# Kernel optimization log

Measured on AMD Instinct MI355X. Metric: run time of the kernel, lower is better.

The kernel has to match this reference:

```python
import jax, jax.numpy as jnp
import numpy as np

DT = 1e-3
TAU_SYN_INV = 50.0   # overridden in SeqNet.__init__
TAU_MEM_INV = 100.0  # norse default
V_TH = 1.0
EPS = 1e-5
H1 = 512
H2 = 512
NOUT = 10


def setup_inputs() -> dict:
    key = jax.random.key(0)
    ks = jax.random.split(key, 11)
    T, B, F = 100, 512, 784
    x = jax.random.normal(ks[0], (T, B, F), dtype=jnp.float32)
    # torch.nn.Linear init ~ U(-1/sqrt(fan_in), 1/sqrt(fan_in))
    def lin(k, out_d, in_d):
        bound = 1.0 / np.sqrt(in_d)
        kw, kb = jax.random.split(k)
        W = jax.random.uniform(kw, (out_d, in_d), jnp.float32, -bound, bound)
        b = jax.random.uniform(kb, (out_d,), jnp.float32, -bound, bound)
        return W, b
    W0, b0 = lin(ks[1], H1, F)
    W1, b1 = lin(ks[2], H2, H1)
    g0 = jnp.ones((H1,), jnp.float32)
    bt0 = jnp.zeros((H1,), jnp.float32)
    g1 = jnp.ones((H2,), jnp.float32)
    bt1 = jnp.zeros((H2,), jnp.float32)
    # norse LILinearCell: input_weights ~ randn / sqrt(hidden), no bias
    Wo = jax.random.normal(ks[3], (NOUT, H2), jnp.float32) / np.sqrt(H2)
    return {"x": x, "W0": W0, "b0": b0, "W1": W1, "b1": b1,
            "g0": g0, "bt0": bt0, "g1": g1, "bt1": bt1, "Wo": Wo}


def _bn(z, g, b):
    # BatchNorm1d in training mode: per-step batch statistics (biased var)
    m = jnp.mean(z, axis=0)
    v = jnp.var(z, axis=0)
    return g * (z - m) * jax.lax.rsqrt(v + EPS) + b


def _lif_step(v, i, cur):
    # norse lif_feed_forward_step, v_leak=0, v_reset=0
    v_dec = v + DT * TAU_MEM_INV * (-v + i)          # membrane decay + input current
    i_dec = i * (1.0 - DT * TAU_SYN_INV)             # synaptic decay
    z = (v_dec - V_TH > 0).astype(cur.dtype)         # heaviside spike
    v_new = (1.0 - z) * v_dec                        # reset to 0 on spike
    i_new = i_dec + cur                              # inject weighted input
    return z, v_new, i_new


def reference(x, W0, b0, W1, b1, g0, bt0, g1, bt1, Wo):
    T, B = x.shape[0], x.shape[1]
    xf = x.reshape(T, B, -1)

    def step(carry, xt):
        v0, i0, v1, i1, vo, io = carry
        cur0 = xt @ W0.T + b0                        # [B, H1]
        z0, v0, i0 = _lif_step(v0, i0, cur0)
        h0 = _bn(z0, g0, bt0)
        cur1 = h0 @ W1.T + b1                        # [B, H2]
        z1, v1, i1 = _lif_step(v1, i1, cur1)
        h1 = _bn(z1, g1, bt1)
        # norse LILinearCell (li_step): leaky integrator, returns v
        vo_new = vo + DT * TAU_MEM_INV * (-vo + io)  # [B, 10]
        io_new = io * (1.0 - DT * TAU_SYN_INV) + h1 @ Wo.T
        return (v0, i0, v1, i1, vo_new, io_new), vo_new

    z32 = lambda d: jnp.zeros((B, d), x.dtype)
    carry0 = (z32(W0.shape[0]), z32(W0.shape[0]),
              z32(W1.shape[0]), z32(W1.shape[0]),
              z32(Wo.shape[0]), z32(Wo.shape[0]))
    _, voltages = jax.lax.scan(step, carry0, xf)
    return voltages  # [T, B, 10]
```

## Files before the change

kernel.cpp:

```cpp
#include <hip/hip_runtime.h>
#include <stdint.h>

#define T_    100
#define B_    512
#define F_    784
#define FP_   800
#define H_    512
#define NOUT_ 10
#define R_    (T_*B_)
#define BH    (B_*H_)

typedef _Float16 f16x8 __attribute__((ext_vector_type(8)));
typedef float    f32x4 __attribute__((ext_vector_type(4)));

__device__ __forceinline__ void gload_lds16(const void* g, void* l) {
    __builtin_amdgcn_global_load_lds(
        (const __attribute__((address_space(1))) uint32_t*)g,
        (__attribute__((address_space(3))) uint32_t*)l, 16, 0, 0);
}

__global__ void convW_kernel(const float* __restrict__ W, _Float16* __restrict__ Wh,
                             _Float16* __restrict__ Wl, int K, int Kp, int n)
{
    int idx = blockIdx.x * 256 + threadIdx.x;
    if (idx >= n) return;
    int r = idx / Kp, k = idx - r * Kp;
    float v = (k < K) ? W[r * K + k] : 0.f;
    _Float16 h = (_Float16)v;
    Wh[idx] = h;
    Wl[idx] = (_Float16)(v - (float)h);
}

__global__ __launch_bounds__(256, 2) void gemm0_mfma(
    const float* __restrict__ X, const _Float16* __restrict__ Wh,
    const _Float16* __restrict__ Wl, const float* __restrict__ bias,
    float* __restrict__ C)
{
    __shared__ _Float16 L[2 * 4 * 4096];
    const int tid  = threadIdx.x;
    const int gl   = (blockIdx.x & 7) * 200 + (blockIdx.x >> 3);
    const int r0   = (gl >> 2) * 128;
    const int n0   = (gl & 3) * 128;
    const int lane = tid & 63;
    const int wm = (tid >> 7) & 1, wn = (tid >> 6) & 1;
    const int frow = lane & 15, fgrp = lane >> 4;

    const int brow = tid >> 2;
    const int bcol = (((tid & 3) ^ ((brow >> 1) & 3)) << 3);
    const _Float16* WhB = Wh + (size_t)(n0 + brow) * FP_ + bcol;
    const _Float16* WlB = Wl + (size_t)(n0 + brow) * FP_ + bcol;

    const int arow = tid >> 1, ahalf = tid & 1;
    const float* Xb = X + (size_t)(r0 + arow) * F_ + ahalf * 16;
    const int aoff = arow * 32;
    const int ac0  = (((ahalf * 2)     ^ ((arow >> 1) & 3)) << 3);
    const int ac1  = (((ahalf * 2 + 1) ^ ((arow >> 1) & 3)) << 3);

    f32x4 acc[4][4];
#pragma unroll
    for (int i = 0; i < 4; i++)
#pragma unroll
        for (int j = 0; j < 4; j++) acc[i][j] = f32x4{0.f, 0.f, 0.f, 0.f};

    auto stageB = [&](int buf, int kt) {
        _Float16* dh = L + buf * 16384 + 8192;
        _Float16* dl = L + buf * 16384 + 12288;
        gload_lds16(WhB + kt,            dh + tid * 8);
        gload_lds16(WhB + 64 * FP_ + kt, dh + 2048 + tid * 8);
        gload_lds16(WlB + kt,            dl + tid * 8);
        gload_lds16(WlB + 64 * FP_ + kt, dl + 2048 + tid * 8);
    };
    auto loadA = [&](float4* xa, int kt) {
#pragma unroll
        for (int j = 0; j < 4; j++) {
            int c = kt + ahalf * 16 + j * 4;
            xa[j] = (c < F_) ? *(const float4*)(Xb + kt + j * 4)
                             : make_float4(0.f, 0.f, 0.f, 0.f);
        }
    };
    auto writeA = [&](const float4* xa, int buf) {
        _Float16* dh = L + buf * 16384;
        _Float16* dl = L + buf * 16384 + 4096;
        const float* v = (const float*)xa;
        f16x8 h0, l0, h1, l1;
#pragma unroll
        for (int j = 0; j < 8; j++) {
            _Float16 a = (_Float16)v[j];
            h0[j] = a; l0[j] = (_Float16)(v[j] - (float)a);
            _Float16 b = (_Float16)v[8 + j];
            h1[j] = b; l1[j] = (_Float16)(v[8 + j] - (float)b);
        }
        *(f16x8*)(dh + aoff + ac0) = h0;
        *(f16x8*)(dh + aoff + ac1) = h1;
        *(f16x8*)(dl + aoff + ac0) = l0;
        *(f16x8*)(dl + aoff + ac1) = l1;
    };

    {
        stageB(0, 0);
        float4 xa[4];
        loadA(xa, 0);
        writeA(xa, 0);
    }
    __syncthreads();

    int cur = 0;
    for (int kt = 0; kt < FP_; kt += 32) {
        const int nxt = cur ^ 1;
        const bool has = (kt + 32) < FP_;
        float4 xa[4];
        if (has) { stageB(nxt, kt + 32); loadA(xa, kt + 32); }

        const _Float16* bp = L + cur * 16384;
        f16x8 ah[4], al[4], bh[4], bl[4];
#pragma unroll
        for (int mi = 0; mi < 4; mi++) {
            int row = wm * 64 + mi * 16 + frow;
            int off = row * 32 + ((fgrp ^ ((row >> 1) & 3)) << 3);
            ah[mi] = *(const f16x8*)(bp + off);
            al[mi] = *(const f16x8*)(bp + 4096 + off);
        }
#pragma unroll
        for (int ni = 0; ni < 4; ni++) {
            int row = wn * 64 + ni * 16 + frow;
            int off = row * 32 + ((fgrp ^ ((row >> 1) & 3)) << 3);
            bh[ni] = *(const f16x8*)(bp + 8192 + off);
            bl[ni] = *(const f16x8*)(bp + 12288 + off);
        }
#pragma unroll
        for (int mi = 0; mi < 4; mi++)
#pragma unroll
            for (int ni = 0; ni < 4; ni++) {
                acc[mi][ni] = __builtin_amdgcn_mfma_f32_16x16x32_f16(ah[mi], bh[ni], acc[mi][ni], 0, 0, 0);
                acc[mi][ni] = __builtin_amdgcn_mfma_f32_16x16x32_f16(ah[mi], bl[ni], acc[mi][ni], 0, 0, 0);
                acc[mi][ni] = __builtin_amdgcn_mfma_f32_16x16x32_f16(al[mi], bh[ni], acc[mi][ni], 0, 0, 0);
            }

        if (has) writeA(xa, nxt);
        __syncthreads();
        cur = nxt;
    }

#pragma unroll
    for (int ni = 0; ni < 4; ni++) {
        int col = n0 + wn * 64 + ni * 16 + frow;
        float bv = bias[col];
#pragma unroll
        for (int mi = 0; mi < 4; mi++) {
            int rbase = r0 + wm * 64 + mi * 16 + fgrp * 4;
#pragma unroll
            for (int p = 0; p < 4; p++)
                C[(size_t)(rbase + p) * H_ + col] = acc[mi][ni][p] + bv;
        }
    }
}

__global__ __launch_bounds__(256, 3) void gemm1_mfma(
    const _Float16* __restrict__ Zh, const float* __restrict__ W1,
    const float* __restrict__ alpha, const float* __restrict__ bW,
    float* __restrict__ C)
{
    __shared__ _Float16 L[2 * 3 * 4096];
    const int tid  = threadIdx.x;
    const int gl   = (blockIdx.x & 7) * 200 + (blockIdx.x >> 3);
    const int r0   = (gl >> 2) * 128;
    const int n0   = (gl & 3) * 128;
    const int tt   = r0 >> 9;
    const int lane = tid & 63;
    const int wm = (tid >> 7) & 1, wn = (tid >> 6) & 1;
    const int frow = lane & 15, fgrp = lane >> 4;

    const int arow = tid >> 2;
    const int acol = (((tid & 3) ^ ((arow >> 1) & 3)) << 3);
    const _Float16* ZhB = Zh + (size_t)(r0 + arow) * H_ + acol;

    const int brow = tid >> 1, bhalf = tid & 1;
    const float* W1B = W1 + (size_t)(n0 + brow) * H_ + bhalf * 16;
    const float* alB = alpha + tt * H_ + bhalf * 16;
    const int boff = brow * 32;
    const int bc0  = (((bhalf * 2)     ^ ((brow >> 1) & 3)) << 3);
    const int bc1  = (((bhalf * 2 + 1) ^ ((brow >> 1) & 3)) << 3);

    f32x4 acc[4][4];
#pragma unroll
    for (int i = 0; i < 4; i++)
#pragma unroll
        for (int j = 0; j < 4; j++) acc[i][j] = f32x4{0.f, 0.f, 0.f, 0.f};

    auto stageA = [&](int buf, int kt) {
        _Float16* d = L + buf * 12288;
        gload_lds16(ZhB + kt,           d + tid * 8);
        gload_lds16(ZhB + 64 * H_ + kt, d + 2048 + tid * 8);
    };
    auto loadB = [&](float4* wv, float4* av, int kt) {
#pragma unroll
        for (int j = 0; j < 4; j++) {
            wv[j] = *(const float4*)(W1B + kt + j * 4);
            av[j] = *(const float4*)(alB + kt + j * 4);
        }
    };
    auto writeB = [&](const float4* wv, const float4* av, int buf) {
        _Float16* dh = L + buf * 12288 + 4096;
        _Float16* dl = L + buf * 12288 + 8192;
        const float* w = (const float*)wv;
        const float* a = (const float*)av;
        f16x8 h0, l0, h1, l1;
#pragma unroll
        for (int j = 0; j < 8; j++) {
            float p0 = a[j] * w[j];
            _Float16 q0 = (_Float16)p0;
            h0[j] = q0; l0[j] = (_Float16)(p0 - (float)q0);
            float p1 = a[8 + j] * w[8 + j];
            _Float16 q1 = (_Float16)p1;
            h1[j] = q1; l1[j] = (_Float16)(p1 - (float)q1);
        }
        *(f16x8*)(dh + boff + bc0) = h0;
        *(f16x8*)(dh + boff + bc1) = h1;
        *(f16x8*)(dl + boff + bc0) = l0;
        *(f16x8*)(dl + boff + bc1) = l1;
    };

    {
        stageA(0, 0);
        float4 wv[4], av[4];
        loadB(wv, av, 0);
        writeB(wv, av, 0);
    }
    __syncthreads();

    int cur = 0;
    for (int kt = 0; kt < H_; kt += 32) {
        const int nxt = cur ^ 1;
        const bool has = (kt + 32) < H_;
        float4 wv[4], av[4];
        if (has) { stageA(nxt, kt + 32); loadB(wv, av, kt + 32); }

        const _Float16* bp = L + cur * 12288;
        f16x8 az[4], bh[4], bl[4];
#pragma unroll
        for (int mi = 0; mi < 4; mi++) {
            int row = wm * 64 + mi * 16 + frow;
            int off = row * 32 + ((fgrp ^ ((row >> 1) & 3)) << 3);
            az[mi] = *(const f16x8*)(bp + off);
        }
#pragma unroll
        for (int ni = 0; ni < 4; ni++) {
            int row = wn * 64 + ni * 16 + frow;
            int off = row * 32 + ((fgrp ^ ((row >> 1) & 3)) << 3);
            bh[ni] = *(const f16x8*)(bp + 4096 + off);
            bl[ni] = *(const f16x8*)(bp + 8192 + off);
        }
#pragma unroll
        for (int mi = 0; mi < 4; mi++)
#pragma unroll
            for (int ni = 0; ni < 4; ni++) {
                acc[mi][ni] = __builtin_amdgcn_mfma_f32_16x16x32_f16(az[mi], bh[ni], acc[mi][ni], 0, 0, 0);
                acc[mi][ni] = __builtin_amdgcn_mfma_f32_16x16x32_f16(az[mi], bl[ni], acc[mi][ni], 0, 0, 0);
            }

        if (has) writeB(wv, av, nxt);
        __syncthreads();
        cur = nxt;
    }

#pragma unroll
    for (int ni = 0; ni < 4; ni++) {
        int col = n0 + wn * 64 + ni * 16 + frow;
        float bv = bW[tt * H_ + col];
#pragma unroll
        for (int mi = 0; mi < 4; mi++) {
            int rbase = r0 + wm * 64 + mi * 16 + fgrp * 4;
#pragma unroll
            for (int p = 0; p < 4; p++)
                C[(size_t)(rbase + p) * H_ + col] = acc[mi][ni][p] + bv;
        }
    }
}

__global__ __launch_bounds__(512) void bw_kernel(
    const float* __restrict__ beta, const float* __restrict__ W1,
    const float* __restrict__ b1, float* __restrict__ bW)
{
    __shared__ float bs[512];
    const int t = blockIdx.x, n = threadIdx.x;
    bs[n] = beta[t * H_ + n];
    __syncthreads();
    const float* wr = W1 + (size_t)n * H_;
    float s = b1[n];
    for (int f = 0; f < H_; f += 4) {
        float4 w = *(const float4*)(wr + f);
        s = fmaf(bs[f],     w.x, s);
        s = fmaf(bs[f + 1], w.y, s);
        s = fmaf(bs[f + 2], w.z, s);
        s = fmaf(bs[f + 3], w.w, s);
    }
    bW[t * H_ + n] = s;
}

__global__ __launch_bounds__(256) void lif_kernel(
    const float* __restrict__ cur, _Float16* __restrict__ z)
{
    const int tid = blockIdx.x * 256 + threadIdx.x;
    float v = 0.f, ii = 0.f;
    const float* p = cur + tid;
    _Float16* q = z + tid;
    for (int t = 0; t < T_; t++) {
        float vd = __fadd_rn(v, __fmul_rn(0.1f, __fsub_rn(ii, v)));
        float id = __fmul_rn(ii, 0.95f);
        int zz = (vd > 1.0f) ? 1 : 0;
        v  = zz ? 0.f : vd;
        ii = __fadd_rn(id, p[(size_t)t * BH]);
        q[(size_t)t * BH] = (_Float16)zz;
    }
}

__global__ void bn_kernel(const _Float16* __restrict__ z,
                          const float* __restrict__ g, const float* __restrict__ bt,
                          float* __restrict__ alpha, float* __restrict__ beta)
{
    const int t = blockIdx.x, h = threadIdx.x;
    const _Float16* p = z + (size_t)t * BH + h;
    float fs = 0.f;
    for (int b = 0; b < B_; b++) fs += (float)p[(size_t)b * H_];
    float m   = fs * (1.0f / 512.0f);
    float var = __fsub_rn(m, __fmul_rn(m, m));
    float al  = g[h] / sqrtf(__fadd_rn(var, 1e-5f));
    float be  = __fsub_rn(bt[h], __fmul_rn(m, al));
    alpha[t * H_ + h] = al;
    beta [t * H_ + h] = be;
}

__global__ __launch_bounds__(256) void ugemm_kernel(
    const _Float16* __restrict__ Z, const float* __restrict__ alpha,
    const float* __restrict__ beta, const float* __restrict__ Wo,
    float* __restrict__ U)
{
    const int tid  = threadIdx.x;
    const int wave = tid >> 6, lane = tid & 63;
    const size_t r = (size_t)blockIdx.x * 4 + wave;
    const int t = (int)(r >> 9);
    const _Float16* zr = Z + r * 512;
    const float* alp = alpha + t * 512;
    const float* bet = beta  + t * 512;
    float acc[NOUT_];
#pragma unroll
    for (int o = 0; o < NOUT_; o++) acc[o] = 0.f;
#pragma unroll
    for (int jj = 0; jj < 8; jj++) {
        int j = jj * 64 + lane;
        float h = fmaf((float)zr[j], alp[j], bet[j]);
#pragma unroll
        for (int o = 0; o < NOUT_; o++) acc[o] = fmaf(h, Wo[o * 512 + j], acc[o]);
    }
#pragma unroll
    for (int o = 0; o < NOUT_; o++) {
        float v = acc[o];
#pragma unroll
        for (int off = 32; off; off >>= 1) v += __shfl_down(v, off, 64);
        if (lane == 0) U[r * NOUT_ + o] = v;
    }
}

__global__ void li_kernel(const float* __restrict__ U, float* __restrict__ out)
{
    const int tid = blockIdx.x * 256 + threadIdx.x;
    if (tid >= B_ * NOUT_) return;
    float vo = 0.f, io = 0.f;
    for (int t = 0; t < T_; t++) {
        vo = __fadd_rn(vo, __fmul_rn(0.1f, __fsub_rn(io, vo)));
        out[t * (B_ * NOUT_) + tid] = vo;
        io = __fadd_rn(__fmul_rn(io, 0.95f), U[t * (B_ * NOUT_) + tid]);
    }
}

extern "C" void kernel_launch(void* const* d_in, const int* in_sizes, int n_in,
                              void* d_out, int out_size, void* d_ws, size_t ws_size,
                              hipStream_t stream)
{
    const float* X   = (const float*)d_in[0];
    const float* W0  = (const float*)d_in[1];
    const float* b0  = (const float*)d_in[2];
    const float* W1  = (const float*)d_in[3];
    const float* b1  = (const float*)d_in[4];
    const float* g0  = (const float*)d_in[5];
    const float* bt0 = (const float*)d_in[6];
    const float* g1  = (const float*)d_in[7];
    const float* bt1 = (const float*)d_in[8];
    const float* Wo  = (const float*)d_in[9];
    float* out = (float*)d_out;

    char* w = (char*)d_ws;
    float*    CUR    = (float*)w;
    _Float16* Zh     = (_Float16*)(w + 104857600);
    float*    alpha0 = (float*)(w + 104857600 + 52428800);
    float*    beta0  = alpha0 + T_*H_;
    float*    alpha1 = beta0  + T_*H_;
    float*    beta1  = alpha1 + T_*H_;
    float*    bW     = beta1  + T_*H_;
    float*    U      = bW     + T_*H_;
    _Float16* W0h    = (_Float16*)(U + R_*NOUT_);
    _Float16* W0l    = W0h + 512*FP_;

    convW_kernel<<<(512*FP_+255)/256, 256, 0, stream>>>(W0, W0h, W0l, F_, FP_, 512*FP_);

    gemm0_mfma  <<<1600,  256, 0, stream>>>(X, W0h, W0l, b0, CUR);
    lif_kernel  <<<1024,  256, 0, stream>>>(CUR, Zh);
    bn_kernel   <<<100,   512, 0, stream>>>(Zh, g0, bt0, alpha0, beta0);
    bw_kernel   <<<100,   512, 0, stream>>>(beta0, W1, b1, bW);
    gemm1_mfma  <<<1600,  256, 0, stream>>>(Zh, W1, alpha0, bW, CUR);
    lif_kernel  <<<1024,  256, 0, stream>>>(CUR, Zh);
    bn_kernel   <<<100,   512, 0, stream>>>(Zh, g1, bt1, alpha1, beta1);
    ugemm_kernel<<<12800, 256, 0, stream>>>(Zh, alpha1, beta1, Wo, U);
    li_kernel   <<<20,    256, 0, stream>>>(U, out);
}
```

Baseline: 605.0 us.

## Triple-buffer async LDS loads in both GEMMs and split BN reduction across blocks

Both MFMA GEMMs now keep three LDS stages for the async-loaded operand and prefetch two k-tiles ahead. Fine-grained vmcnt/lgkmcnt waits and raw s_barrier replace __syncthreads, and the MFMA block runs at raised wave priority, all to hide global-load latency. The batch-norm statistics kernel, which used only 100 blocks, is split into an 800-block partial-sum pass and a small finalize pass to expose more parallelism. The added LDS drops gemm1 occupancy from 3 to 2 blocks per CU, and the hand-written wait counts must exactly match the number of outstanding loads.

```diff
diff --git a/kernel.cpp b/kernel.cpp
--- a/kernel.cpp
+++ b/kernel.cpp
@@ -36,7 +36,7 @@
     const _Float16* __restrict__ Wl, const float* __restrict__ bias,
     float* __restrict__ C)
 {
-    __shared__ _Float16 L[2 * 4 * 4096];
+    __shared__ _Float16 L[40960];
     const int tid  = threadIdx.x;
     const int gl   = (blockIdx.x & 7) * 200 + (blockIdx.x >> 3);
     const int r0   = (gl >> 2) * 128;
@@ -62,15 +62,15 @@
 #pragma unroll
         for (int j = 0; j < 4; j++) acc[i][j] = f32x4{0.f, 0.f, 0.f, 0.f};
 
-    auto stageB = [&](int buf, int kt) {
-        _Float16* dh = L + buf * 16384 + 8192;
-        _Float16* dl = L + buf * 16384 + 12288;
+    auto stageB = [&](int sbuf, int kt) {
+        _Float16* dh = L + 16384 + sbuf * 8192;
+        _Float16* dl = dh + 4096;
         gload_lds16(WhB + kt,            dh + tid * 8);
         gload_lds16(WhB + 64 * FP_ + kt, dh + 2048 + tid * 8);
         gload_lds16(WlB + kt,            dl + tid * 8);
         gload_lds16(WlB + 64 * FP_ + kt, dl + 2048 + tid * 8);
     };
-    auto loadA = [&](float4* xa, int kt) {
+    auto loadA = [&](float4 (&xa)[4], int kt) {
 #pragma unroll
         for (int j = 0; j < 4; j++) {
             int c = kt + ahalf * 16 + j * 4;
@@ -78,9 +78,9 @@
                              : make_float4(0.f, 0.f, 0.f, 0.f);
         }
     };
-    auto writeA = [&](const float4* xa, int buf) {
-        _Float16* dh = L + buf * 16384;
-        _Float16* dl = L + buf * 16384 + 4096;
+    auto writeA = [&](int abuf, const float4 (&xa)[4]) {
+        _Float16* dh = L + abuf * 8192;
+        _Float16* dl = dh + 4096;
         const float* v = (const float*)xa;
         f16x8 h0, l0, h1, l1;
 #pragma unroll
@@ -96,37 +96,38 @@
         *(f16x8*)(dl + aoff + ac1) = l1;
     };
 
-    {
-        stageB(0, 0);
-        float4 xa[4];
-        loadA(xa, 0);
-        writeA(xa, 0);
-    }
-    __syncthreads();
-
-    int cur = 0;
-    for (int kt = 0; kt < FP_; kt += 32) {
-        const int nxt = cur ^ 1;
-        const bool has = (kt + 32) < FP_;
-        float4 xa[4];
-        if (has) { stageB(nxt, kt + 32); loadA(xa, kt + 32); }
-
-        const _Float16* bp = L + cur * 16384;
+    float4 R0[4], R1[4];
+    stageB(0, 0);
+    stageB(1, 32);
+    loadA(R0, 0);
+    loadA(R1, 32);
+    writeA(0, R0);
+    asm volatile("s_waitcnt lgkmcnt(0)" ::: "memory");
+    __builtin_amdgcn_sched_barrier(0);
+    __builtin_amdgcn_s_barrier();
+    __builtin_amdgcn_sched_barrier(0);
+
+    auto body = [&](int k, int rbuf, int sbuf, float4 (&Rl)[4], float4 (&Rw)[4],
+                    bool pf, bool dw) {
+        if (pf) { stageB(sbuf, (k + 2) * 32); loadA(Rl, (k + 2) * 32); }
+        const _Float16* Ab = L + (k & 1) * 8192;
+        const _Float16* Bb = L + 16384 + rbuf * 8192;
         f16x8 ah[4], al[4], bh[4], bl[4];
 #pragma unroll
         for (int mi = 0; mi < 4; mi++) {
             int row = wm * 64 + mi * 16 + frow;
             int off = row * 32 + ((fgrp ^ ((row >> 1) & 3)) << 3);
-            ah[mi] = *(const f16x8*)(bp + off);
-            al[mi] = *(const f16x8*)(bp + 4096 + off);
+            ah[mi] = *(const f16x8*)(Ab + off);
+            al[mi] = *(const f16x8*)(Ab + 4096 + off);
         }
 #pragma unroll
         for (int ni = 0; ni < 4; ni++) {
             int row = wn * 64 + ni * 16 + frow;
             int off = row * 32 + ((fgrp ^ ((row >> 1) & 3)) << 3);
-            bh[ni] = *(const f16x8*)(bp + 8192 + off);
-            bl[ni] = *(const f16x8*)(bp + 12288 + off);
-        }
+            bh[ni] = *(const f16x8*)(Bb + off);
+            bl[ni] = *(const f16x8*)(Bb + 4096 + off);
+        }
+        __builtin_amdgcn_s_setprio(1);
 #pragma unroll
         for (int mi = 0; mi < 4; mi++)
 #pragma unroll
@@ -135,11 +136,24 @@
                 acc[mi][ni] = __builtin_amdgcn_mfma_f32_16x16x32_f16(ah[mi], bl[ni], acc[mi][ni], 0, 0, 0);
                 acc[mi][ni] = __builtin_amdgcn_mfma_f32_16x16x32_f16(al[mi], bh[ni], acc[mi][ni], 0, 0, 0);
             }
-
-        if (has) writeA(xa, nxt);
-        __syncthreads();
-        cur = nxt;
-    }
+        __builtin_amdgcn_s_setprio(0);
+        if (dw) writeA((k + 1) & 1, Rw);
+        asm volatile("s_waitcnt vmcnt(8)" ::: "memory");
+        asm volatile("s_waitcnt lgkmcnt(0)" ::: "memory");
+        __builtin_amdgcn_sched_barrier(0);
+        __builtin_amdgcn_s_barrier();
+        __builtin_amdgcn_sched_barrier(0);
+    };
+
+    int rb = 0;
+    for (int kp = 0; kp < 12; kp++) {
+        int k = kp * 2;
+        body(k,     rb, rb == 0 ? 2 : rb - 1, R0, R1, (k + 2) <= 24, true);
+        rb = (rb == 2) ? 0 : rb + 1;
+        body(k + 1, rb, rb == 0 ? 2 : rb - 1, R1, R0, (k + 3) <= 24, true);
+        rb = (rb == 2) ? 0 : rb + 1;
+    }
+    body(24, rb, 0, R0, R1, false, false);
 
 #pragma unroll
     for (int ni = 0; ni < 4; ni++) {
@@ -155,12 +169,12 @@
     }
 }
 
-__global__ __launch_bounds__(256, 3) void gemm1_mfma(
+__global__ __launch_bounds__(256, 2) void gemm1_mfma(
     const _Float16* __restrict__ Zh, const float* __restrict__ W1,
     const float* __restrict__ alpha, const float* __restrict__ bW,
     float* __restrict__ C)
 {
-    __shared__ _Float16 L[2 * 3 * 4096];
+    __shared__ _Float16 L[28672];
     const int tid  = threadIdx.x;
     const int gl   = (blockIdx.x & 7) * 200 + (blockIdx.x >> 3);
     const int r0   = (gl >> 2) * 128;
@@ -187,21 +201,21 @@
 #pragma unroll
         for (int j = 0; j < 4; j++) acc[i][j] = f32x4{0.f, 0.f, 0.f, 0.f};
 
-    auto stageA = [&](int buf, int kt) {
-        _Float16* d = L + buf * 12288;
+    auto stageA = [&](int sbuf, int kt) {
+        _Float16* d = L + sbuf * 4096;
         gload_lds16(ZhB + kt,           d + tid * 8);
         gload_lds16(ZhB + 64 * H_ + kt, d + 2048 + tid * 8);
     };
-    auto loadB = [&](float4* wv, float4* av, int kt) {
+    auto loadB = [&](float4 (&wv)[4], float4 (&av)[4], int kt) {
 #pragma unroll
         for (int j = 0; j < 4; j++) {
             wv[j] = *(const float4*)(W1B + kt + j * 4);
             av[j] = *(const float4*)(alB + kt + j * 4);
         }
     };
-    auto writeB = [&](const float4* wv, const float4* av, int buf) {
-        _Float16* dh = L + buf * 12288 + 4096;
-        _Float16* dl = L + buf * 12288 + 8192;
+    auto writeB = [&](int wbuf, const float4 (&wv)[4], const float4 (&av)[4]) {
+        _Float16* dh = L + 12288 + wbuf * 8192;
+        _Float16* dl = dh + 4096;
         const float* w = (const float*)wv;
         const float* a = (const float*)av;
         f16x8 h0, l0, h1, l1;
@@ -220,36 +234,37 @@
         *(f16x8*)(dl + boff + bc1) = l1;
     };
 
-    {
-        stageA(0, 0);
-        float4 wv[4], av[4];
-        loadB(wv, av, 0);
-        writeB(wv, av, 0);
-    }
-    __syncthreads();
-
-    int cur = 0;
-    for (int kt = 0; kt < H_; kt += 32) {
-        const int nxt = cur ^ 1;
-        const bool has = (kt + 32) < H_;
-        float4 wv[4], av[4];
-        if (has) { stageA(nxt, kt + 32); loadB(wv, av, kt + 32); }
-
-        const _Float16* bp = L + cur * 12288;
+    float4 Wv0[4], Av0[4], Wv1[4], Av1[4];
+    stageA(0, 0);
+    stageA(1, 32);
+    loadB(Wv0, Av0, 0);
+    loadB(Wv1, Av1, 32);
+    writeB(0, Wv0, Av0);
+    asm volatile("s_waitcnt lgkmcnt(0)" ::: "memory");
+    __builtin_amdgcn_sched_barrier(0);
+    __builtin_amdgcn_s_barrier();
+    __builtin_amdgcn_sched_barrier(0);
+
+    auto body = [&](int k, int rbuf, int sbuf, float4 (&Wl_)[4], float4 (&Al_)[4],
+                    float4 (&Ww_)[4], float4 (&Aw_)[4], bool pf, bool dw) {
+        if (pf) { stageA(sbuf, (k + 2) * 32); loadB(Wl_, Al_, (k + 2) * 32); }
+        const _Float16* Ab = L + rbuf * 4096;
+        const _Float16* Bb = L + 12288 + (k & 1) * 8192;
         f16x8 az[4], bh[4], bl[4];
 #pragma unroll
         for (int mi = 0; mi < 4; mi++) {
             int row = wm * 64 + mi * 16 + frow;
             int off = row * 32 + ((fgrp ^ ((row >> 1) & 3)) << 3);
-            az[mi] = *(const f16x8*)(bp + off);
+            az[mi] = *(const f16x8*)(Ab + off);
         }
 #pragma unroll
         for (int ni = 0; ni < 4; ni++) {
             int row = wn * 64 + ni * 16 + frow;
             int off = row * 32 + ((fgrp ^ ((row >> 1) & 3)) << 3);
-            bh[ni] = *(const f16x8*)(bp + 4096 + off);
-            bl[ni] = *(const f16x8*)(bp + 8192 + off);
-        }
+            bh[ni] = *(const f16x8*)(Bb + off);
+            bl[ni] = *(const f16x8*)(Bb + 4096 + off);
+        }
+        __builtin_amdgcn_s_setprio(1);
 #pragma unroll
         for (int mi = 0; mi < 4; mi++)
 #pragma unroll
@@ -257,11 +272,26 @@
                 acc[mi][ni] = __builtin_amdgcn_mfma_f32_16x16x32_f16(az[mi], bh[ni], acc[mi][ni], 0, 0, 0);
                 acc[mi][ni] = __builtin_amdgcn_mfma_f32_16x16x32_f16(az[mi], bl[ni], acc[mi][ni], 0, 0, 0);
             }
-
-        if (has) writeB(wv, av, nxt);
-        __syncthreads();
-        cur = nxt;
-    }
+        __builtin_amdgcn_s_setprio(0);
+        if (dw) writeB((k + 1) & 1, Ww_, Aw_);
+        asm volatile("s_waitcnt vmcnt(10)" ::: "memory");
+        asm volatile("s_waitcnt lgkmcnt(0)" ::: "memory");
+        __builtin_amdgcn_sched_barrier(0);
+        __builtin_amdgcn_s_barrier();
+        __builtin_amdgcn_sched_barrier(0);
+    };
+
+    int rb = 0;
+    for (int kp = 0; kp < 7; kp++) {
+        int k = kp * 2;
+        body(k,     rb, rb == 0 ? 2 : rb - 1, Wv0, Av0, Wv1, Av1, true, true);
+        rb = (rb == 2) ? 0 : rb + 1;
+        body(k + 1, rb, rb == 0 ? 2 : rb - 1, Wv1, Av1, Wv0, Av0, (k + 3) <= 15, true);
+        rb = (rb == 2) ? 0 : rb + 1;
+    }
+    body(14, rb, 0, Wv0, Av0, Wv1, Av1, false, true);
+    rb = 0;
+    body(15, rb, 0, Wv1, Av1, Wv0, Av0, false, false);
 
 #pragma unroll
     for (int ni = 0; ni < 4; ni++) {
@@ -314,14 +344,24 @@
     }
 }
 
-__global__ void bn_kernel(const _Float16* __restrict__ z,
+__global__ __launch_bounds__(512) void bn_part(const _Float16* __restrict__ z,
+                                               float* __restrict__ part)
+{
+    const int t = blockIdx.x >> 3, c = blockIdx.x & 7, h = threadIdx.x;
+    const _Float16* p = z + (size_t)t * BH + (size_t)(c * 64) * H_ + h;
+    float fs = 0.f;
+    for (int b = 0; b < 64; b++) fs += (float)p[(size_t)b * H_];
+    part[(size_t)blockIdx.x * H_ + h] = fs;
+}
+
+__global__ __launch_bounds__(512) void bn_fin(const float* __restrict__ part,
                           const float* __restrict__ g, const float* __restrict__ bt,
                           float* __restrict__ alpha, float* __restrict__ beta)
 {
     const int t = blockIdx.x, h = threadIdx.x;
-    const _Float16* p = z + (size_t)t * BH + h;
     float fs = 0.f;
-    for (int b = 0; b < B_; b++) fs += (float)p[(size_t)b * H_];
+#pragma unroll
+    for (int c = 0; c < 8; c++) fs += part[(size_t)(t * 8 + c) * H_ + h];
     float m   = fs * (1.0f / 512.0f);
     float var = __fsub_rn(m, __fmul_rn(m, m));
     float al  = g[h] / sqrtf(__fadd_rn(var, 1e-5f));
@@ -400,16 +440,19 @@
     float*    U      = bW     + T_*H_;
     _Float16* W0h    = (_Float16*)(U + R_*NOUT_);
     _Float16* W0l    = W0h + 512*FP_;
+    float*    part   = (float*)(W0l + 512*FP_);
 
     convW_kernel<<<(512*FP_+255)/256, 256, 0, stream>>>(W0, W0h, W0l, F_, FP_, 512*FP_);
 
     gemm0_mfma  <<<1600,  256, 0, stream>>>(X, W0h, W0l, b0, CUR);
     lif_kernel  <<<1024,  256, 0, stream>>>(CUR, Zh);
-    bn_kernel   <<<100,   512, 0, stream>>>(Zh, g0, bt0, alpha0, beta0);
+    bn_part     <<<800,   512, 0, stream>>>(Zh, part);
+    bn_fin      <<<100,   512, 0, stream>>>(part, g0, bt0, alpha0, beta0);
     bw_kernel   <<<100,   512, 0, stream>>>(beta0, W1, b1, bW);
     gemm1_mfma  <<<1600,  256, 0, stream>>>(Zh, W1, alpha0, bW, CUR);
     lif_kernel  <<<1024,  256, 0, stream>>>(CUR, Zh);
-    bn_kernel   <<<100,   512, 0, stream>>>(Zh, g1, bt1, alpha1, beta1);
+    bn_part     <<<800,   512, 0, stream>>>(Zh, part);
+    bn_fin      <<<100,   512, 0, stream>>>(part, g1, bt1, alpha1, beta1);
     ugemm_kernel<<<12800, 256, 0, stream>>>(Zh, alpha1, beta1, Wo, U);
     li_kernel   <<<20,    256, 0, stream>>>(U, out);
 }
```

Result: faster. 590.7 us (-2.4%).
